# Optimization experiments

Hardware: AMD Instinct MI355X
Metric: run time of the kernel (lower is better)

## Reference

```python
import jax, jax.numpy as jnp
import numpy as np

UNITS = 50257
CUTOFF = [2000, 10000, UNITS]  # _cutoff = cutoff + [units]
C = 1024                        # channels (d_model)
N = 4096                        # flattened tokens (batch*seq)
N_TAILS = len(CUTOFF) - 1       # 2
ROOT_OUT = CUTOFF[0] + N_TAILS  # 2002
TAIL_DIMS = [256, 64]           # round(C/4**(i+1)/8)*8


def setup_inputs() -> dict:
    key = jax.random.key(0)
    ks = jax.random.split(key, 7)
    logits = jax.random.normal(ks[0], (N, C), jnp.float32)
    targets = jax.random.randint(ks[1], (N,), 0, UNITS, jnp.int32)
    s = 0.02
    head_kernel = jax.random.normal(ks[2], (C, ROOT_OUT), jnp.float32) * s
    proj0 = jax.random.normal(ks[3], (C, TAIL_DIMS[0]), jnp.float32) * s
    scale0 = jax.random.normal(ks[4], (TAIL_DIMS[0], CUTOFF[1] - CUTOFF[0]), jnp.float32) * s
    proj1 = jax.random.normal(ks[5], (C, TAIL_DIMS[1]), jnp.float32) * s
    scale1 = jax.random.normal(ks[6], (TAIL_DIMS[1], CUTOFF[2] - CUTOFF[1]), jnp.float32) * s
    return {"logits": logits, "targets": targets, "head_kernel": head_kernel,
            "proj0": proj0, "scale0": scale0, "proj1": proj1, "scale1": scale1}


def _sparse_ce(lg, labels):
    # sparse softmax cross entropy, numerically stable (single logsumexp)
    lse = jax.nn.logsumexp(lg, axis=-1)
    picked = jnp.take_along_axis(lg, labels[:, None].astype(jnp.int32), axis=1)[:, 0]
    return lse - picked


def reference(logits, targets, head_kernel, proj0, scale0, proj1, scale1):
    # Faithful jax version of AdaptiveSoftmax._train_loss (return_probs=False,
    # dropout=0, no bias on Denses, loss_reduction=SUM_OVER_BATCH_SIZE i.e. mean).
    # Dynamic boolean gather is replaced by dense compute + masked mean, which
    # yields identical math under jit (mean over the routed subset).
    root_logits = (logits @ head_kernel).astype(jnp.float32)  # [N, ROOT_OUT]
    root_targets = targets
    tails = [(proj0, scale0), (proj1, scale1)]
    losses = []
    for i, (p, s) in enumerate(tails):
        lo, hi = CUTOFF[i], CUTOFF[i + 1]
        m = (targets >= lo) & (targets < hi)
        root_targets = jnp.where(m, CUTOFF[0] + i, root_targets)
        tail_logits = ((logits @ p) @ s).astype(jnp.float32)  # [N, hi-lo]
        tail_tgt = jnp.clip(targets - lo, 0, hi - lo - 1)
        ce = _sparse_ce(tail_logits, tail_tgt)
        mf = m.astype(jnp.float32)
        losses.append(jnp.sum(ce * mf) / jnp.maximum(jnp.sum(mf), 1.0))
    root_loss = jnp.mean(_sparse_ce(root_logits, root_targets))
    all_losses = jnp.stack([root_loss] + losses)
    return jnp.mean(all_losses)
```

## Files before the change

### kernel.cpp

```cpp
#include <hip/hip_runtime.h>
#include <math.h>
#include <stdint.h>

#define NROWS 4096
#define CDIM 1024
#define T0_LO 2000
#define T0_HI 10000
#define T1_LO 10000
#define ROOT_COLS 2002
#define ROOT_PAD 2048
#define T0_COLS 8000
#define T0_PAD 8064
#define T1_COLS 40257
#define T1_PAD 40320
#define HB_STRIDE 320
#define LOG2E 1.44269504088896340736f
#define LN2 0.69314718055994530942f

using short8  = __attribute__((ext_vector_type(8))) short;
using ushort8 = __attribute__((ext_vector_type(8))) unsigned short;
using floatx4 = __attribute__((ext_vector_type(4))) float;

__device__ __forceinline__ unsigned short f2bf(float x) {
  union { float f; unsigned int u; } v; v.f = x;
  unsigned int r = v.u + 0x7fffu + ((v.u >> 16) & 1u);
  return (unsigned short)(r >> 16);
}
__device__ __forceinline__ float bf2f(unsigned short h) {
  union { unsigned int u; float f; } v; v.u = ((unsigned int)h) << 16;
  return v.f;
}
__device__ __forceinline__ floatx4 mfma16(short8 a, short8 b, floatx4 c) {
  return __builtin_amdgcn_mfma_f32_16x16x32_bf16(a, b, c, 0, 0, 0);
}
__device__ __forceinline__ void stage16(const unsigned short* g,
                                        unsigned short* lds_wave_base, int lane) {
#if __has_builtin(__builtin_amdgcn_global_load_lds)
  __builtin_amdgcn_global_load_lds(
      (const __attribute__((address_space(1))) void*)g,
      (__attribute__((address_space(3))) void*)lds_wave_base, 16, 0, 0);
#else
  ((ushort8*)lds_wave_base)[lane] = *(const ushort8*)g;
#endif
}

static constexpr size_t B_HB  = 0;
static constexpr size_t B_LB  = B_HB + 4096ull * 320 * 2;
static constexpr size_t B_WP  = B_LB + 4096ull * 1024 * 2;
static constexpr size_t B_WH  = B_WP + 384ull * 1024 * 2;
static constexpr size_t B_WS0 = B_WH + 2048ull * 1024 * 2;
static constexpr size_t B_WS1 = B_WS0 + 8064ull * 256 * 2;
static constexpr size_t B_S   = B_WS1 + 40320ull * 64 * 2;
static constexpr size_t B_P   = B_S + 3ull * 4096 * 4;
static constexpr size_t B_I0  = B_P + 3ull * 4096 * 4;
static constexpr size_t B_I1  = B_I0 + 4096ull * 4;
static constexpr size_t B_CNT = B_I1 + 4096ull * 4;


struct TInfo {
  const float* W; unsigned short* Wt;
  int K, N, Npad, nx, rel, mode;
  float scale;
};

__device__ __forceinline__ TInfo tp_resolve(
    int tg, const float* head, const float* scale0, const float* scale1,
    const float* proj0, const float* proj1, unsigned short* Wh,
    unsigned short* Ws0, unsigned short* Ws1, unsigned short* Wp) {
  TInfo ti;
  if (tg < 2048)      { ti.W = head;   ti.Wt = Wh;  ti.K = 1024; ti.N = ROOT_COLS; ti.Npad = ROOT_PAD; ti.nx = 64;   ti.rel = tg;        ti.mode = 1; ti.scale = LOG2E; }
  else if (tg < 4064) { ti.W = scale0; ti.Wt = Ws0; ti.K = 256;  ti.N = T0_COLS;   ti.Npad = T0_PAD;   ti.nx = 252;  ti.rel = tg - 2048; ti.mode = 0; ti.scale = LOG2E; }
  else if (tg < 6584) { ti.W = scale1; ti.Wt = Ws1; ti.K = 64;   ti.N = T1_COLS;   ti.Npad = T1_PAD;   ti.nx = 1260; ti.rel = tg - 4064; ti.mode = 2; ti.scale = LOG2E; }
  else if (tg < 6840) { ti.W = proj0;  ti.Wt = Wp;  ti.K = 1024; ti.N = 256;       ti.Npad = 256;      ti.nx = 8;    ti.rel = tg - 6584; ti.mode = 0; ti.scale = 1.f; }
  else                { ti.W = proj1;  ti.Wt = Wp + 256 * 1024; ti.K = 1024; ti.N = 64; ti.Npad = 64; ti.nx = 2; ti.rel = tg - 6840; ti.mode = 0; ti.scale = 1.f; }
  return ti;
}

__device__ __forceinline__ float4 tp_load(const TInfo& ti, int tid) {
  const int n0 = (ti.rel % ti.nx) * 32, k0 = (ti.rel / ti.nx) * 32;
  float4 v = make_float4(0.f, 0.f, 0.f, 0.f);
  if (ti.mode == 0) {
    const int lk = tid >> 3, ln = (tid & 7) << 2;
    const int n = n0 + ln;
    if (n + 3 < ti.N) v = *(const float4*)(ti.W + (size_t)(k0 + lk) * ti.N + n);
  } else if (ti.mode == 1) {
    const int lk = tid >> 4, ln = (tid & 15) << 1;
    const int n = n0 + ln;
    if (n + 1 < ti.N) {
      float2 a = *(const float2*)(ti.W + (size_t)(k0 + lk) * ti.N + n);
      float2 b = *(const float2*)(ti.W + (size_t)(k0 + lk + 16) * ti.N + n);
      v = make_float4(a.x, a.y, b.x, b.y);
    }
  } else {
    const int tx = tid & 31, ty = tid >> 5;
    const int n = n0 + tx;
    if (n < ti.N) {
      v.x = ti.W[(size_t)(k0 + ty) * ti.N + n];
      v.y = ti.W[(size_t)(k0 + ty + 8) * ti.N + n];
      v.z = ti.W[(size_t)(k0 + ty + 16) * ti.N + n];
      v.w = ti.W[(size_t)(k0 + ty + 24) * ti.N + n];
    }
  }
  return v;
}

__device__ __forceinline__ void tp_wlds(const TInfo& ti, int tid, float4 v,
                                        float (*tile)[33]) {
  const float s = ti.scale;
  if (ti.mode == 0) {
    const int lk = tid >> 3, ln = (tid & 7) << 2;
    tile[lk][ln] = v.x * s; tile[lk][ln + 1] = v.y * s;
    tile[lk][ln + 2] = v.z * s; tile[lk][ln + 3] = v.w * s;
  } else if (ti.mode == 1) {
    const int lk = tid >> 4, ln = (tid & 15) << 1;
    tile[lk][ln] = v.x * s; tile[lk][ln + 1] = v.y * s;
    tile[lk + 16][ln] = v.z * s; tile[lk + 16][ln + 1] = v.w * s;
  } else {
    const int tx = tid & 31, ty = tid >> 5;
    tile[ty][tx] = v.x * s; tile[ty + 8][tx] = v.y * s;
    tile[ty + 16][tx] = v.z * s; tile[ty + 24][tx] = v.w * s;
  }
}

__device__ __forceinline__ void tp_store(const TInfo& ti, int tid,
                                         float (*tile)[33]) {
  if (tid < 128) {
    const int n0 = (ti.rel % ti.nx) * 32, k0 = (ti.rel / ti.nx) * 32;
    const int nloc = tid >> 2, kg = tid & 3;
    const int n = n0 + nloc;
    if (n < ti.Npad) {
      ushort8 x;
#pragma unroll
      for (int j = 0; j < 8; j++) x[j] = f2bf(tile[kg * 8 + j][nloc]);
      *(ushort8*)&ti.Wt[(size_t)n * ti.K + k0 + kg * 8] = x;
    }
  }
}

#define PT_NT       1726
#define PP_LB_END   (PT_NT + 2048)
#define PP_ZERO_END (PP_LB_END + 32)
#define PP_S_END    (PP_ZERO_END + 4)
#define PP_TOTAL    (PP_S_END + 1)

__global__ __launch_bounds__(256) void prep_kernel(
    const float* __restrict__ head, const float* __restrict__ proj0,
    const float* __restrict__ proj1, const float* __restrict__ scale0,
    const float* __restrict__ scale1, const float* __restrict__ logits,
    const int* __restrict__ targets,
    unsigned short* __restrict__ Wh, unsigned short* __restrict__ Wp,
    unsigned short* __restrict__ Ws0, unsigned short* __restrict__ Ws1,
    unsigned short* __restrict__ Lb, float* __restrict__ S,
    int* __restrict__ idx0, int* __restrict__ idx1, int* __restrict__ cnt) {
  __shared__ float bufs[2][32][33];
  const int id = blockIdx.x, tid = threadIdx.x;
  if (id < PT_NT) {
    TInfo ti0 = tp_resolve(id * 4 + 0, head, scale0, scale1, proj0, proj1, Wh, Ws0, Ws1, Wp);
    TInfo ti1 = tp_resolve(id * 4 + 1, head, scale0, scale1, proj0, proj1, Wh, Ws0, Ws1, Wp);
    TInfo ti2 = tp_resolve(id * 4 + 2, head, scale0, scale1, proj0, proj1, Wh, Ws0, Ws1, Wp);
    TInfo ti3 = tp_resolve(id * 4 + 3, head, scale0, scale1, proj0, proj1, Wh, Ws0, Ws1, Wp);
    float4 rv = tp_load(ti0, tid);
    tp_wlds(ti0, tid, rv, bufs[0]);
    rv = tp_load(ti1, tid);
    __syncthreads();
    tp_store(ti0, tid, bufs[0]);
    tp_wlds(ti1, tid, rv, bufs[1]);
    rv = tp_load(ti2, tid);
    __syncthreads();
    tp_store(ti1, tid, bufs[1]);
    tp_wlds(ti2, tid, rv, bufs[0]);
    rv = tp_load(ti3, tid);
    __syncthreads();
    tp_store(ti2, tid, bufs[0]);
    tp_wlds(ti3, tid, rv, bufs[1]);
    __syncthreads();
    tp_store(ti3, tid, bufs[1]);
    return;
  }
  if (id < PP_LB_END) {
    size_t base = (size_t)(id - PT_NT) * 2048 + tid * 8;
    float4 v0 = *(const float4*)(logits + base);
    float4 v1 = *(const float4*)(logits + base + 4);
    ushort8 h;
    h[0] = f2bf(v0.x); h[1] = f2bf(v0.y); h[2] = f2bf(v0.z); h[3] = f2bf(v0.w);
    h[4] = f2bf(v1.x); h[5] = f2bf(v1.y); h[6] = f2bf(v1.z); h[7] = f2bf(v1.w);
    *(ushort8*)(Lb + base) = h;
    return;
  }
  if (id < PP_ZERO_END) {
    size_t off = (size_t)(id - PP_LB_END) * 2048 + tid * 8;
    ushort8 z = {0, 0, 0, 0, 0, 0, 0, 0};
    *(ushort8*)(Wp + 320ull * 1024 + off) = z;
    return;
  }
  if (id < PP_S_END) {
    int rel = id - PP_ZERO_END;
    float4 z = make_float4(0.f, 0.f, 0.f, 0.f);
#pragma unroll
    for (int j = 0; j < 3; j++)
      ((float4*)S)[rel * 768 + j * 256 + tid] = z;
    return;
  }
  int* base2 = (int*)&bufs[0][0][0];
  if (tid < 2) base2[tid] = 0;
  __syncthreads();
  for (int n = tid; n < NROWS; n += 256) {
    int t = targets[n];
    if (t >= T0_LO && t < T0_HI) idx0[atomicAdd(&base2[0], 1)] = n;
    else if (t >= T1_LO)         idx1[atomicAdd(&base2[1], 1)] = n;
  }
  __syncthreads();
  if (tid < 2) cnt[tid] = base2[tid];
}

template<int CI>
__device__ __forceinline__ void gemm64_kloop(
    unsigned short* A_lds,
    const unsigned short* Arow,
    const unsigned short* const (&Bbase)[CI],
    floatx4 (&acc)[CI][4], int tid) {
  const int lane = tid & 63, w = tid >> 6;
  const int m = lane & 15, quad = lane >> 4, keym = m & 7;
  int goff[4];
#pragma unroll
  for (int it = 0; it < 4; it++) {
    int s = w * 256 + it * 64 + lane;
    int r = s >> 4, p = s & 15;
    int cq = p ^ (r & 7);
    goff[it] = r * CDIM + cq * 8;
  }
#pragma unroll
  for (int it = 0; it < 4; it++)
    stage16(Arow + goff[it], &A_lds[(w * 256 + it * 64) * 8], lane);
  for (int h = 0; h < 8; h++) {
    unsigned short* cur = A_lds + (h & 1) * (64 * 128);
    unsigned short* nxt = A_lds + ((h + 1) & 1) * (64 * 128);
    __syncthreads();
    if (h + 1 < 8) {
#pragma unroll
      for (int it = 0; it < 4; it++)
        stage16(Arow + goff[it] + (h + 1) * 128,
                &nxt[(w * 256 + it * 64) * 8], lane);
    }
    short8 b[CI][4];
#pragma unroll
    for (int ci = 0; ci < CI; ci++)
#pragma unroll
      for (int ks = 0; ks < 4; ks++)
        b[ci][ks] = *(const short8*)(Bbase[ci] + h * 128 + ks * 32);
    short8 areg[4][4];
#pragma unroll
    for (int t = 0; t < 4; t++)
#pragma unroll
      for (int ks = 0; ks < 4; ks++) {
        int ch = ((ks << 2) + quad) ^ keym;
        areg[t][ks] = *(const short8*)&cur[(t * 16 + m) * 128 + (ch << 3)];
      }
#pragma unroll
    for (int ci = 0; ci < CI; ci++)
#pragma unroll
      for (int ks = 0; ks < 4; ks++)
#pragma unroll
        for (int t = 0; t < 4; t++)
          acc[ci][t] = mfma16(areg[t][ks], b[ci][ks], acc[ci][t]);
  }
}

__global__ __launch_bounds__(256) void hidden_kernel(
    const unsigned short* __restrict__ Lb,
    const unsigned short* __restrict__ Wp,
    unsigned short* __restrict__ Hb) {
  __shared__ unsigned short A_lds[64 * 256];
  const int id = blockIdx.x, tid = threadIdx.x;
  const int xcd = id & 7, k = id >> 3;
  const int row0 = (xcd * 8 + (k & 7)) * 64;
  const int cg0 = k >> 3;
  const int lane = tid & 63, w = tid >> 6;
  const int m = lane & 15, quad = lane >> 4;
  const floatx4 zf = {0.f, 0.f, 0.f, 0.f};
  floatx4 acc[1][4];
#pragma unroll
  for (int t = 0; t < 4; t++) acc[0][t] = zf;
  const unsigned short* Bb[1] = {
      Wp + (size_t)(cg0 * 64 + w * 16 + m) * CDIM + quad * 8};
  gemm64_kloop<1>(A_lds, Lb + (size_t)row0 * CDIM, Bb, acc, tid);
  int n = cg0 * 64 + w * 16 + m;
  if (n < HB_STRIDE) {
#pragma unroll
    for (int t = 0; t < 4; t++)
#pragma unroll
      for (int r = 0; r < 4; r++)
        Hb[(size_t)(row0 + t * 16 + quad * 4 + r) * HB_STRIDE + n] =
            f2bf(acc[0][t][r]);
  }
}

#define MG_ROOT 512
#define MG_T1   480
#define MG_T0   2688
#define MG_PICK 1024
#define MG_TOTAL (MG_ROOT + MG_T1 + MG_T0 + MG_PICK)

__device__ __forceinline__ void root_compute(
    const unsigned short* cur, const short8 (&b)[2][2], floatx4 (&acc)[2][8],
    int m, int quad, int keym) {
#pragma unroll
  for (int hf = 0; hf < 2; hf++) {
    short8 areg[4][2];
#pragma unroll
    for (int t = 0; t < 4; t++)
#pragma unroll
      for (int ks = 0; ks < 2; ks++) {
        int ch = ((ks << 2) + quad) ^ keym;
        areg[t][ks] = *(const short8*)&cur[(hf * 64 + t * 16 + m) * 64 + (ch << 3)];
      }
#pragma unroll
    for (int ci = 0; ci < 2; ci++)
#pragma unroll
      for (int ks = 0; ks < 2; ks++)
#pragma unroll
        for (int t = 0; t < 4; t++)
          acc[ci][hf * 4 + t] = mfma16(areg[t][ks], b[ci][ks], acc[ci][hf * 4 + t]);
  }
}

__device__ __forceinline__ void root_stage(
    const unsigned short* Arow, const int (&goff)[4], int koff,
    unsigned short* buf, int w, int lane) {
#pragma unroll
  for (int it = 0; it < 4; it++)
    stage16(Arow + goff[it] + koff, &buf[(it * 256 + w * 64) * 8], lane);
}

__device__ __forceinline__ void root_loadB(
    const unsigned short* const (&Bb)[2], int koff, short8 (&b)[2][2]) {
#pragma unroll
  for (int ci = 0; ci < 2; ci++)
#pragma unroll
    for (int ks = 0; ks < 2; ks++)
      b[ci][ks] = *(const short8*)(Bb[ci] + koff + ks * 32);
}

__device__ __forceinline__ void root_path(
    unsigned char* smem, int bx, int by,
    const unsigned short* __restrict__ Lb,
    const unsigned short* __restrict__ Wh, float* __restrict__ S) {
  unsigned short* bufA = (unsigned short*)smem;
  unsigned short* bufB = bufA + 128 * 64;
  const int tid = threadIdx.x;
  const int row0 = bx * 128;
  const int cg0 = by * 2;
  const int lane = tid & 63, w = tid >> 6;
  const int m = lane & 15, quad = lane >> 4, keym = m & 7;
  const floatx4 zf = {0.f, 0.f, 0.f, 0.f};
  floatx4 acc[2][8];
#pragma unroll
  for (int ci = 0; ci < 2; ci++)
#pragma unroll
    for (int t = 0; t < 8; t++) acc[ci][t] = zf;
  const unsigned short* Bb[2] = {
      Wh + (size_t)((cg0 + 0) * 64 + w * 16 + m) * CDIM + quad * 8,
      Wh + (size_t)((cg0 + 1) * 64 + w * 16 + m) * CDIM + quad * 8};
  const unsigned short* Arow = Lb + (size_t)row0 * CDIM;
  int goff[4];
#pragma unroll
  for (int it = 0; it < 4; it++) {
    int s = it * 256 + w * 64 + lane;
    int r = s >> 3, p = s & 7;
    int cq = p ^ (r & 7);
    goff[it] = r * CDIM + cq * 8;
  }
  short8 b0[2][2], b1[2][2];
  root_stage(Arow, goff, 0, bufA, w, lane);
  root_loadB(Bb, 0, b0);
  for (int hh = 0; hh < 8; hh++) {
    __syncthreads();
    root_stage(Arow, goff, (hh * 2 + 1) * 64, bufB, w, lane);
    root_loadB(Bb, (hh * 2 + 1) * 64, b1);
    root_compute(bufA, b0, acc, m, quad, keym);
    __syncthreads();
    if (hh < 7) {
      root_stage(Arow, goff, (hh * 2 + 2) * 64, bufA, w, lane);
      root_loadB(Bb, (hh * 2 + 2) * 64, b0);
    }
    root_compute(bufB, b1, acc, m, quad, keym);
  }
  __syncthreads();
  float* sums = (float*)smem;
  if (tid < 128) sums[tid] = 0.f;
  __syncthreads();
#pragma unroll
  for (int t = 0; t < 8; t++)
#pragma unroll
    for (int r = 0; r < 4; r++) {
      float e = __builtin_amdgcn_exp2f(acc[0][t][r]) +
                __builtin_amdgcn_exp2f(acc[1][t][r]);
      e += __shfl_xor(e, 1); e += __shfl_xor(e, 2);
      e += __shfl_xor(e, 4); e += __shfl_xor(e, 8);
      if (m == 0)
        atomicAdd(&sums[(t >> 2) * 64 + (t & 3) * 16 + quad * 4 + r], e);
    }
  __syncthreads();
  if (tid < 128) atomicAdd(&S[row0 + tid], sums[tid]);
}

template<int K, int TILES, int MODE>
__device__ __forceinline__ void tail_path(
    unsigned char* smem, int bx, int by,
    const unsigned short* __restrict__ Hb, int acol0,
    const unsigned short* __restrict__ Wt, int ncgpb,
    const int* __restrict__ idx, const int* __restrict__ cnt,
    float* __restrict__ S) {
  constexpr int BM = TILES * 16;
  constexpr int CpR = K / 8;
  constexpr int KS = K / 32;
  unsigned short* A_lds = (unsigned short*)smem;
  int* row_lds = (int*)(smem + (size_t)BM * K * 2);
  float* sum_lds = (float*)(smem + (size_t)BM * K * 2 + BM * 4);
  const int tid = threadIdx.x;
  const int count = cnt[MODE - 1];
  const int row0 = bx * BM;
  if (row0 >= count) return;
  if (tid < BM) {
    int r = row0 + tid;
    row_lds[tid] = (r < count) ? idx[r] : -1;
    sum_lds[tid] = 0.f;
  }
  __syncthreads();
#pragma unroll
  for (int i = 0; i < BM * CpR / 256; i++) {
    int c = tid + 256 * i;
    int rl = c / CpR, cq = c % CpR;
    int row = row_lds[rl];
    ushort8 v = {0, 0, 0, 0, 0, 0, 0, 0};
    if (row >= 0) v = *(const ushort8*)(Hb + (size_t)row * HB_STRIDE + acol0 + cq * 8);
    *(ushort8*)&A_lds[rl * K + ((cq ^ (rl & 7)) << 3)] = v;
  }
  __syncthreads();
  const int lane = tid & 63, w = tid >> 6;
  const int m = lane & 15, quad = lane >> 4, keym = m & 7;
  const floatx4 zf = {0.f, 0.f, 0.f, 0.f};
  short8 areg[TILES][KS];
#pragma unroll
  for (int t = 0; t < TILES; t++)
#pragma unroll
    for (int ks = 0; ks < KS; ks++) {
      int ch = ((ks << 2) + quad) ^ keym;
      areg[t][ks] = *(const short8*)&A_lds[(t * 16 + m) * K + (ch << 3)];
    }
  float runsum[TILES][4];
#pragma unroll
  for (int t = 0; t < TILES; t++)
#pragma unroll
    for (int r = 0; r < 4; r++) runsum[t][r] = 0.f;

  const int cg0 = by * ncgpb;
  const unsigned short* Bp = Wt + (size_t)(cg0 * 64 + w * 16 + m) * K + quad * 8;
  short8 b0[KS], b1[KS];
#pragma unroll
  for (int ks = 0; ks < KS; ks++) b0[ks] = *(const short8*)(Bp + ks * 32);
#pragma unroll
  for (int ks = 0; ks < KS; ks++)
    b1[ks] = *(const short8*)(Bp + (size_t)64 * K + ks * 32);

  for (int cc = 0; cc < ncgpb; cc += 2) {
    floatx4 acc[TILES];
#pragma unroll
    for (int t = 0; t < TILES; t++) acc[t] = zf;
#pragma unroll
    for (int ks = 0; ks < KS; ks++)
#pragma unroll
      for (int t = 0; t < TILES; t++) acc[t] = mfma16(areg[t][ks], b0[ks], acc[t]);
    if (cc + 2 < ncgpb) {
      const unsigned short* p = Bp + (size_t)(cc + 2) * 64 * K;
#pragma unroll
      for (int ks = 0; ks < KS; ks++) b0[ks] = *(const short8*)(p + ks * 32);
    }
#pragma unroll
    for (int t = 0; t < TILES; t++)
#pragma unroll
      for (int r = 0; r < 4; r++)
        runsum[t][r] += __builtin_amdgcn_exp2f(acc[t][r]);

#pragma unroll
    for (int t = 0; t < TILES; t++) acc[t] = zf;
#pragma unroll
    for (int ks = 0; ks < KS; ks++)
#pragma unroll
      for (int t = 0; t < TILES; t++) acc[t] = mfma16(areg[t][ks], b1[ks], acc[t]);
    if (cc + 3 < ncgpb) {
      const unsigned short* p = Bp + (size_t)(cc + 3) * 64 * K;
#pragma unroll
      for (int ks = 0; ks < KS; ks++) b1[ks] = *(const short8*)(p + ks * 32);
    }
#pragma unroll
    for (int t = 0; t < TILES; t++)
#pragma unroll
      for (int r = 0; r < 4; r++)
        runsum[t][r] += __builtin_amdgcn_exp2f(acc[t][r]);
  }

#pragma unroll
  for (int t = 0; t < TILES; t++)
#pragma unroll
    for (int r = 0; r < 4; r++) {
      float e = runsum[t][r];
      e += __shfl_xor(e, 1); e += __shfl_xor(e, 2);
      e += __shfl_xor(e, 4); e += __shfl_xor(e, 8);
      if (m == 0) atomicAdd(&sum_lds[t * 16 + quad * 4 + r], e);
    }
  __syncthreads();
  if (tid < BM) {
    int row = row_lds[tid];
    if (row >= 0) atomicAdd(&S[row], sum_lds[tid]);
  }
}

__device__ __forceinline__ void picked_path(
    int rel, const float* __restrict__ logits, const int* __restrict__ targets,
    const unsigned short* __restrict__ Wh,
    const unsigned short* __restrict__ Ws0,
    const unsigned short* __restrict__ Ws1,
    const unsigned short* __restrict__ Hb, float* __restrict__ P) {
  const int tid = threadIdx.x, lane = tid & 63;
  const int row = rel * 4 + (tid >> 6);
  const int t = targets[row];
  const int tr = (t >= T0_LO && t < T0_HI) ? T0_LO : ((t >= T1_LO) ? T0_LO + 1 : t);
  const float* a = logits + (size_t)row * CDIM + lane * 16;
  const unsigned short* wr = Wh + (size_t)tr * CDIM + lane * 16;
  float acc = 0.f;
#pragma unroll
  for (int q = 0; q < 2; q++) {
    ushort8 wv = *(const ushort8*)(wr + q * 8);
    float4 a0 = ((const float4*)a)[q * 2];
    float4 a1 = ((const float4*)a)[q * 2 + 1];
    acc += a0.x * bf2f(wv[0]) + a0.y * bf2f(wv[1]) + a0.z * bf2f(wv[2]) + a0.w * bf2f(wv[3]);
    acc += a1.x * bf2f(wv[4]) + a1.y * bf2f(wv[5]) + a1.z * bf2f(wv[6]) + a1.w * bf2f(wv[7]);
  }
#pragma unroll
  for (int off = 1; off < 64; off <<= 1) acc += __shfl_xor(acc, off);
  if (lane == 0) P[row] = acc * LN2;
  if (t >= T0_LO) {
    float acc2 = 0.f;
    if (t < T0_HI) {
      const unsigned short* h = Hb + (size_t)row * HB_STRIDE + lane * 4;
      const unsigned short* w2 = Ws0 + (size_t)(t - T0_LO) * 256 + lane * 4;
#pragma unroll
      for (int j = 0; j < 4; j++) acc2 += bf2f(h[j]) * bf2f(w2[j]);
    } else {
      acc2 = bf2f(Hb[(size_t)row * HB_STRIDE + 256 + lane]) *
             bf2f(Ws1[(size_t)(t - T1_LO) * 64 + lane]);
    }
#pragma unroll
    for (int off = 1; off < 64; off <<= 1) acc2 += __shfl_xor(acc2, off);
    if (lane == 0) P[(t < T0_HI ? NROWS : 2 * NROWS) + row] = acc2 * LN2;
  }
}

__global__ __launch_bounds__(256, 2) void mega_kernel(
    const unsigned short* __restrict__ Lb,
    const unsigned short* __restrict__ Wh,
    const unsigned short* __restrict__ Ws0,
    const unsigned short* __restrict__ Ws1,
    const unsigned short* __restrict__ Hb,
    const float* __restrict__ logits, const int* __restrict__ targets,
    const int* __restrict__ idx0, const int* __restrict__ idx1,
    const int* __restrict__ cnt, float* __restrict__ S, float* __restrict__ P) {
  __shared__ __align__(16) unsigned char smem[32768];
  int bid = blockIdx.x;
  if (bid < MG_ROOT) {
    int wk = ((bid & 7) << 6) + (bid >> 3);
    root_path(smem, wk >> 4, wk & 15, Lb, Wh, S);
    return;
  }
  bid -= MG_ROOT;
  if (bid < MG_T1) {
    int wk = (bid & 7) * 60 + (bid >> 3);
    tail_path<64, 8, 2>(smem, wk & 31, wk >> 5, Hb, 256, Ws1, 42, idx1, cnt,
                        S + 2 * NROWS);
    return;
  }
  bid -= MG_T1;
  if (bid < MG_T0) {
    int wk = (bid & 7) * 336 + (bid >> 3);
    tail_path<256, 2, 1>(smem, wk & 127, wk >> 7, Hb, 0, Ws0, 6, idx0, cnt,
                         S + NROWS);
    return;
  }
  bid -= MG_T0;
  picked_path(bid, logits, targets, Wh, Ws0, Ws1, Hb, P);
}

__global__ __launch_bounds__(1024) void loss_kernel(
    const int* __restrict__ targets,
    const float* __restrict__ S,
    const float* __restrict__ P,
    float* __restrict__ out) {
  const int tid = threadIdx.x;
  float sr = 0.f, s0 = 0.f, s1 = 0.f, c0 = 0.f, c1 = 0.f;
  for (int n = tid; n < NROWS; n += 1024) {
    int t = targets[n];
    sr += logf(S[n] - 46.f) - P[n];
    if (t >= T0_LO && t < T0_HI) { s0 += logf(S[NROWS + n] - 64.f) - P[NROWS + n]; c0 += 1.f; }
    else if (t >= T1_LO)         { s1 += logf(S[2 * NROWS + n] - 63.f) - P[2 * NROWS + n]; c1 += 1.f; }
  }
  for (int off = 32; off > 0; off >>= 1) {
    sr += __shfl_down(sr, off);
    s0 += __shfl_down(s0, off);
    s1 += __shfl_down(s1, off);
    c0 += __shfl_down(c0, off);
    c1 += __shfl_down(c1, off);
  }
  __shared__ float red[16][5];
  int wv = tid >> 6;
  if ((tid & 63) == 0) { red[wv][0] = sr; red[wv][1] = s0; red[wv][2] = s1; red[wv][3] = c0; red[wv][4] = c1; }
  __syncthreads();
  if (tid == 0) {
    sr = 0.f; s0 = 0.f; s1 = 0.f; c0 = 0.f; c1 = 0.f;
#pragma unroll
    for (int i = 0; i < 16; i++) {
      sr += red[i][0]; s0 += red[i][1]; s1 += red[i][2];
      c0 += red[i][3]; c1 += red[i][4];
    }
    float root_loss = sr / (float)NROWS;
    float l0 = s0 / fmaxf(c0, 1.f);
    float l1 = s1 / fmaxf(c1, 1.f);
    out[0] = (root_loss + l0 + l1) / 3.f;
  }
}

extern "C" void kernel_launch(void* const* d_in, const int* in_sizes, int n_in,
                              void* d_out, int out_size, void* d_ws, size_t ws_size,
                              hipStream_t stream) {
  const float* logits  = (const float*)d_in[0];
  const int*   targets = (const int*)d_in[1];
  const float* head    = (const float*)d_in[2];
  const float* proj0   = (const float*)d_in[3];
  const float* scale0  = (const float*)d_in[4];
  const float* proj1   = (const float*)d_in[5];
  const float* scale1  = (const float*)d_in[6];
  float* out = (float*)d_out;
  char* ws = (char*)d_ws;

  unsigned short* Hb  = (unsigned short*)(ws + B_HB);
  unsigned short* Lb  = (unsigned short*)(ws + B_LB);
  unsigned short* Wp  = (unsigned short*)(ws + B_WP);
  unsigned short* Wh  = (unsigned short*)(ws + B_WH);
  unsigned short* Ws0 = (unsigned short*)(ws + B_WS0);
  unsigned short* Ws1 = (unsigned short*)(ws + B_WS1);
  float* S = (float*)(ws + B_S);
  float* P = (float*)(ws + B_P);
  int* idx0 = (int*)(ws + B_I0);
  int* idx1 = (int*)(ws + B_I1);
  int* cnt  = (int*)(ws + B_CNT);

  prep_kernel<<<PP_TOTAL, 256, 0, stream>>>(head, proj0, proj1, scale0, scale1,
                                            logits, targets, Wh, Wp, Ws0, Ws1,
                                            Lb, S, idx0, idx1, cnt);
  hidden_kernel<<<320, 256, 0, stream>>>(Lb, Wp, Hb);
  mega_kernel<<<MG_TOTAL, 256, 0, stream>>>(Lb, Wh, Ws0, Ws1, Hb, logits,
                                            targets, idx0, idx1, cnt, S, P);
  loss_kernel<<<1, 1024, 0, stream>>>(targets, S, P, out);
}
```

Baseline: 184.1 us.

## Fuse root picked-logit into root GEMM epilogue and size tail0 work to routed count

The root-path GEMM epilogue now reads each row's routed target and writes the picked root logit directly from the accumulator. This removes the separate fp32 dot product over logits in the picked path, which now handles only tail targets. The tail-0 GEMM switches from a fixed grid of 2688 blocks to 672 persistent blocks that loop over only the row tiles covering the routed count, so fully empty tiles are skipped. The picked-path block order is also swizzled. The picked root logit now comes from bf16 activations instead of fp32 logits, which slightly changes precision, and the persistent loop adds a sync per work item.

```diff
diff --git a/kernel.cpp b/kernel.cpp
--- a/kernel.cpp
+++ b/kernel.cpp
@@ -55,7 +55,6 @@
 static constexpr size_t B_I0  = B_P + 3ull * 4096 * 4;
 static constexpr size_t B_I1  = B_I0 + 4096ull * 4;
 static constexpr size_t B_CNT = B_I1 + 4096ull * 4;
-
 
 struct TInfo {
   const float* W; unsigned short* Wt;
@@ -297,9 +296,9 @@
 
 #define MG_ROOT 512
 #define MG_T1   480
-#define MG_T0   2688
+#define MG_T0N  672
 #define MG_PICK 1024
-#define MG_TOTAL (MG_ROOT + MG_T1 + MG_T0 + MG_PICK)
+#define MG_TOTAL (MG_ROOT + MG_T1 + MG_T0N + MG_PICK)
 
 __device__ __forceinline__ void root_compute(
     const unsigned short* cur, const short8 (&b)[2][2], floatx4 (&acc)[2][8],
@@ -344,7 +343,9 @@
 __device__ __forceinline__ void root_path(
     unsigned char* smem, int bx, int by,
     const unsigned short* __restrict__ Lb,
-    const unsigned short* __restrict__ Wh, float* __restrict__ S) {
+    const unsigned short* __restrict__ Wh,
+    const int* __restrict__ targets,
+    float* __restrict__ S, float* __restrict__ P) {
   unsigned short* bufA = (unsigned short*)smem;
   unsigned short* bufB = bufA + 128 * 64;
   const int tid = threadIdx.x;
@@ -387,18 +388,28 @@
   }
   __syncthreads();
   float* sums = (float*)smem;
-  if (tid < 128) sums[tid] = 0.f;
-  __syncthreads();
+  int* tr_lds = (int*)(smem + 512);
+  if (tid < 128) {
+    sums[tid] = 0.f;
+    int t = targets[row0 + tid];
+    tr_lds[tid] = (t >= T0_LO && t < T0_HI) ? T0_LO
+                                            : ((t >= T1_LO) ? T0_LO + 1 : t);
+  }
+  __syncthreads();
+  const int col0 = cg0 * 64 + w * 16 + m;
 #pragma unroll
   for (int t = 0; t < 8; t++)
 #pragma unroll
     for (int r = 0; r < 4; r++) {
+      int row = (t >> 2) * 64 + (t & 3) * 16 + quad * 4 + r;
+      int trow = tr_lds[row];
+      if (trow == col0)      P[row0 + row] = acc[0][t][r] * LN2;
+      if (trow == col0 + 64) P[row0 + row] = acc[1][t][r] * LN2;
       float e = __builtin_amdgcn_exp2f(acc[0][t][r]) +
                 __builtin_amdgcn_exp2f(acc[1][t][r]);
       e += __shfl_xor(e, 1); e += __shfl_xor(e, 2);
       e += __shfl_xor(e, 4); e += __shfl_xor(e, 8);
-      if (m == 0)
-        atomicAdd(&sums[(t >> 2) * 64 + (t & 3) * 16 + quad * 4 + r], e);
+      if (m == 0) atomicAdd(&sums[row], e);
     }
   __syncthreads();
   if (tid < 128) atomicAdd(&S[row0 + tid], sums[tid]);
@@ -517,44 +528,27 @@
 }
 
 __device__ __forceinline__ void picked_path(
-    int rel, const float* __restrict__ logits, const int* __restrict__ targets,
-    const unsigned short* __restrict__ Wh,
+    int rel, const int* __restrict__ targets,
     const unsigned short* __restrict__ Ws0,
     const unsigned short* __restrict__ Ws1,
     const unsigned short* __restrict__ Hb, float* __restrict__ P) {
   const int tid = threadIdx.x, lane = tid & 63;
   const int row = rel * 4 + (tid >> 6);
   const int t = targets[row];
-  const int tr = (t >= T0_LO && t < T0_HI) ? T0_LO : ((t >= T1_LO) ? T0_LO + 1 : t);
-  const float* a = logits + (size_t)row * CDIM + lane * 16;
-  const unsigned short* wr = Wh + (size_t)tr * CDIM + lane * 16;
-  float acc = 0.f;
-#pragma unroll
-  for (int q = 0; q < 2; q++) {
-    ushort8 wv = *(const ushort8*)(wr + q * 8);
-    float4 a0 = ((const float4*)a)[q * 2];
-    float4 a1 = ((const float4*)a)[q * 2 + 1];
-    acc += a0.x * bf2f(wv[0]) + a0.y * bf2f(wv[1]) + a0.z * bf2f(wv[2]) + a0.w * bf2f(wv[3]);
-    acc += a1.x * bf2f(wv[4]) + a1.y * bf2f(wv[5]) + a1.z * bf2f(wv[6]) + a1.w * bf2f(wv[7]);
-  }
-#pragma unroll
-  for (int off = 1; off < 64; off <<= 1) acc += __shfl_xor(acc, off);
-  if (lane == 0) P[row] = acc * LN2;
-  if (t >= T0_LO) {
-    float acc2 = 0.f;
-    if (t < T0_HI) {
-      const unsigned short* h = Hb + (size_t)row * HB_STRIDE + lane * 4;
-      const unsigned short* w2 = Ws0 + (size_t)(t - T0_LO) * 256 + lane * 4;
-#pragma unroll
-      for (int j = 0; j < 4; j++) acc2 += bf2f(h[j]) * bf2f(w2[j]);
-    } else {
-      acc2 = bf2f(Hb[(size_t)row * HB_STRIDE + 256 + lane]) *
-             bf2f(Ws1[(size_t)(t - T1_LO) * 64 + lane]);
-    }
-#pragma unroll
-    for (int off = 1; off < 64; off <<= 1) acc2 += __shfl_xor(acc2, off);
-    if (lane == 0) P[(t < T0_HI ? NROWS : 2 * NROWS) + row] = acc2 * LN2;
-  }
+  if (t < T0_LO) return;
+  float acc2 = 0.f;
+  if (t < T0_HI) {
+    const unsigned short* h = Hb + (size_t)row * HB_STRIDE + lane * 4;
+    const unsigned short* w2 = Ws0 + (size_t)(t - T0_LO) * 256 + lane * 4;
+#pragma unroll
+    for (int j = 0; j < 4; j++) acc2 += bf2f(h[j]) * bf2f(w2[j]);
+  } else {
+    acc2 = bf2f(Hb[(size_t)row * HB_STRIDE + 256 + lane]) *
+           bf2f(Ws1[(size_t)(t - T1_LO) * 64 + lane]);
+  }
+#pragma unroll
+  for (int off = 1; off < 64; off <<= 1) acc2 += __shfl_xor(acc2, off);
+  if (lane == 0) P[(t < T0_HI ? NROWS : 2 * NROWS) + row] = acc2 * LN2;
 }
 
 __global__ __launch_bounds__(256, 2) void mega_kernel(
@@ -563,14 +557,14 @@
     const unsigned short* __restrict__ Ws0,
     const unsigned short* __restrict__ Ws1,
     const unsigned short* __restrict__ Hb,
-    const float* __restrict__ logits, const int* __restrict__ targets,
+    const int* __restrict__ targets,
     const int* __restrict__ idx0, const int* __restrict__ idx1,
     const int* __restrict__ cnt, float* __restrict__ S, float* __restrict__ P) {
   __shared__ __align__(16) unsigned char smem[32768];
   int bid = blockIdx.x;
   if (bid < MG_ROOT) {
     int wk = ((bid & 7) << 6) + (bid >> 3);
-    root_path(smem, wk >> 4, wk & 15, Lb, Wh, S);
+    root_path(smem, wk >> 4, wk & 15, Lb, Wh, targets, S, P);
     return;
   }
   bid -= MG_ROOT;
@@ -581,14 +575,20 @@
     return;
   }
   bid -= MG_T1;
-  if (bid < MG_T0) {
-    int wk = (bid & 7) * 336 + (bid >> 3);
-    tail_path<256, 2, 1>(smem, wk & 127, wk >> 7, Hb, 0, Ws0, 6, idx0, cnt,
-                         S + NROWS);
+  if (bid < MG_T0N) {
+    int rel = (bid & 7) * 84 + (bid >> 3);
+    int count = cnt[0];
+    int nx = (count + 31) >> 5;
+    int nworks = nx * 21;
+    for (int wk = rel; wk < nworks; wk += MG_T0N) {
+      __syncthreads();
+      tail_path<256, 2, 1>(smem, wk % nx, wk / nx, Hb, 0, Ws0, 6, idx0, cnt,
+                           S + NROWS);
+    }
     return;
   }
-  bid -= MG_T0;
-  picked_path(bid, logits, targets, Wh, Ws0, Ws1, Hb, P);
+  bid -= MG_T0N;
+  picked_path((bid & 7) * 128 + (bid >> 3), targets, Ws0, Ws1, Hb, P);
 }
 
 __global__ __launch_bounds__(1024) void loss_kernel(
@@ -658,7 +658,7 @@
                                             logits, targets, Wh, Wp, Ws0, Ws1,
                                             Lb, S, idx0, idx1, cnt);
   hidden_kernel<<<320, 256, 0, stream>>>(Lb, Wp, Hb);
-  mega_kernel<<<MG_TOTAL, 256, 0, stream>>>(Lb, Wh, Ws0, Ws1, Hb, logits,
-                                            targets, idx0, idx1, cnt, S, P);
+  mega_kernel<<<MG_TOTAL, 256, 0, stream>>>(Lb, Wh, Ws0, Ws1, Hb, targets,
+                                            idx0, idx1, cnt, S, P);
   loss_kernel<<<1, 1024, 0, stream>>>(targets, S, P, out);
 }
```

Measured after the change: 189.0 us. 2.6% more time.

## Fuse hidden projection into mega kernel using ticketed blocks and a device-wide counter

Applied to the files above, without the earlier changes.

Removes the separate hidden_kernel launch. Each mega_kernel block now takes an atomic ticket, and the first 320 tickets compute a hidden-projection tile, then bump a completion counter. Root-path blocks, which do not need Hb, proceed right away. Tail and picked blocks spin with s_sleep until all 320 hidden tiles are done. This aims to overlap the hidden GEMM with the root GEMM and to save one launch boundary, at the cost of spin-waiting and a sync counter that lives in the padding of the Wp workspace and relies on being reset each call.

```diff
diff --git a/kernel.cpp b/kernel.cpp
--- a/kernel.cpp
+++ b/kernel.cpp
@@ -55,7 +55,7 @@
 static constexpr size_t B_I0  = B_P + 3ull * 4096 * 4;
 static constexpr size_t B_I1  = B_I0 + 4096ull * 4;
 static constexpr size_t B_CNT = B_I1 + 4096ull * 4;
-
+#define HSYNC_USHORT_OFF (336 * 1024)
 
 struct TInfo {
   const float* W; unsigned short* Wt;
@@ -266,14 +266,14 @@
   }
 }
 
-__global__ __launch_bounds__(256) void hidden_kernel(
+__device__ __forceinline__ void hidden_block(
+    int id, int tid, unsigned char* smem,
     const unsigned short* __restrict__ Lb,
     const unsigned short* __restrict__ Wp,
     unsigned short* __restrict__ Hb) {
-  __shared__ unsigned short A_lds[64 * 256];
-  const int id = blockIdx.x, tid = threadIdx.x;
-  const int xcd = id & 7, k = id >> 3;
-  const int row0 = (xcd * 8 + (k & 7)) * 64;
+  unsigned short* A_lds = (unsigned short*)smem;
+  const int g = id & 7, k = id >> 3;
+  const int row0 = (g * 8 + (k & 7)) * 64;
   const int cg0 = k >> 3;
   const int lane = tid & 63, w = tid >> 6;
   const int m = lane & 15, quad = lane >> 4;
@@ -562,17 +562,34 @@
     const unsigned short* __restrict__ Wh,
     const unsigned short* __restrict__ Ws0,
     const unsigned short* __restrict__ Ws1,
-    const unsigned short* __restrict__ Hb,
+    const unsigned short* __restrict__ Wp,
+    unsigned short* __restrict__ Hb,
     const float* __restrict__ logits, const int* __restrict__ targets,
     const int* __restrict__ idx0, const int* __restrict__ idx1,
-    const int* __restrict__ cnt, float* __restrict__ S, float* __restrict__ P) {
+    const int* __restrict__ cnt, int* __restrict__ hsync,
+    float* __restrict__ S, float* __restrict__ P) {
   __shared__ __align__(16) unsigned char smem[32768];
+  __shared__ int tkt_s;
+  const int tid = threadIdx.x;
+  if (tid == 0) tkt_s = atomicAdd(&hsync[0], 1);
+  __syncthreads();
+  const int tkt = tkt_s;
+  if (tkt < 320) {
+    hidden_block(tkt, tid, smem, Lb, Wp, Hb);
+    __syncthreads();
+    if (tid == 0) { __threadfence(); atomicAdd(&hsync[1], 1); }
+  }
   int bid = blockIdx.x;
   if (bid < MG_ROOT) {
     int wk = ((bid & 7) << 6) + (bid >> 3);
     root_path(smem, wk >> 4, wk & 15, Lb, Wh, S);
     return;
   }
+  if (tid == 0) {
+    while (atomicAdd(&hsync[1], 0) < 320) __builtin_amdgcn_s_sleep(8);
+  }
+  __syncthreads();
+  __threadfence();
   bid -= MG_ROOT;
   if (bid < MG_T1) {
     int wk = (bid & 7) * 60 + (bid >> 3);
@@ -653,12 +670,13 @@
   int* idx0 = (int*)(ws + B_I0);
   int* idx1 = (int*)(ws + B_I1);
   int* cnt  = (int*)(ws + B_CNT);
+  int* hsync = (int*)(ws + B_WP + (size_t)HSYNC_USHORT_OFF * 2);
 
   prep_kernel<<<PP_TOTAL, 256, 0, stream>>>(head, proj0, proj1, scale0, scale1,
                                             logits, targets, Wh, Wp, Ws0, Ws1,
                                             Lb, S, idx0, idx1, cnt);
-  hidden_kernel<<<320, 256, 0, stream>>>(Lb, Wp, Hb);
-  mega_kernel<<<MG_TOTAL, 256, 0, stream>>>(Lb, Wh, Ws0, Ws1, Hb, logits,
-                                            targets, idx0, idx1, cnt, S, P);
+  mega_kernel<<<MG_TOTAL, 256, 0, stream>>>(Lb, Wh, Ws0, Ws1, Wp, Hb, logits,
+                                            targets, idx0, idx1, cnt, hsync,
+                                            S, P);
   loss_kernel<<<1, 1024, 0, stream>>>(targets, S, P, out);
 }
```

After: 575.0 us. 3.12x slower.
